# Kernel tuning notes

Measured on AMD Instinct MI355X. Metric: run time of the kernel, lower is better.

Reference implementation:

```python
import jax, jax.numpy as jnp
import numpy as np

D_MODEL = 1024
N_HEADS = 16
D_HEAD = D_MODEL // N_HEADS          # 64
ROT_DIM = D_HEAD // 2                # 32, rotary dim (lucidrains dim arg)
THETA = 10000.0
BATCH, SEQ = 4, 4096


def _rope(t):
    """lucidrains rotate_queries_or_keys with seq_dim=-2, applied to t of shape (H,B,dh,S).
    Positions run along the dh axis (size D_HEAD); rotation touches only the first
    ROT_DIM entries of the last axis (S); the rest passes through unchanged."""
    inv_freq = 1.0 / (THETA ** (jnp.arange(0, ROT_DIM, 2, dtype=jnp.float32) / ROT_DIM))  # (ROT_DIM//2,)
    pos = jnp.arange(D_HEAD, dtype=jnp.float32)                                           # (dh,)
    freqs = pos[:, None] * inv_freq[None, :]                                              # (dh, ROT_DIM//2)
    freqs = jnp.repeat(freqs, 2, axis=-1)                                                 # (dh, ROT_DIM) interleaved f0,f0,f1,f1
    cos, sin = jnp.cos(freqs), jnp.sin(freqs)                                             # broadcast over (H,B,dh,ROT_DIM)
    t_rot, t_pass = t[..., :ROT_DIM], t[..., ROT_DIM:]
    x1, x2 = t_rot[..., 0::2], t_rot[..., 1::2]
    rot_half = jnp.stack((-x2, x1), axis=-1).reshape(t_rot.shape)                         # rotate_half (adjacent pairs)
    t_rot = t_rot * cos + rot_half * sin
    return jnp.concatenate([t_rot, t_pass], axis=-1)


def setup_inputs() -> dict:
    key = jax.random.key(0)
    k1, k2, k3 = jax.random.split(key, 3)
    x = jax.random.normal(k1, (BATCH, SEQ, D_MODEL), jnp.float32)
    W = jax.random.normal(k2, (3 * D_MODEL, D_MODEL), jnp.float32) * (D_MODEL ** -0.5)  # torch Linear weight layout
    b = jax.random.normal(k3, (3 * D_MODEL,), jnp.float32) * 0.01
    return {"x": x, "W": W, "b": b}


def reference(x, W, b):
    B, S, _ = x.shape
    qkv = x @ W.T + b                                            # (B,S,3D)
    qkv = qkv.reshape(B, S, N_HEADS, 3 * D_HEAD).transpose(2, 0, 3, 1)  # (H,B,3dh,S)
    q, k, v = jnp.split(qkv, 3, axis=-2)                         # each (H,B,dh,S)
    q = _rope(q)
    k = _rope(k)
    scale = D_HEAD ** -0.5
    scores = jnp.einsum('hbds,hbes->hbde', q, k) * scale         # (H,B,dh,dh) — contracts over S
    probs = jax.nn.softmax(scores, axis=-1)
    out = jnp.einsum('hbde,hbes->hbds', probs, v)                # (H,B,dh,S)
    out = out.transpose(0, 2, 1, 3).reshape(B, S, N_HEADS * D_HEAD)  # faithful to torch transpose(1,2).reshape
    return out
```

## Files before the change

### kernel.cpp

```cpp
#include <hip/hip_runtime.h>
#include <stdint.h>

#define D_MODEL 1024
#define N_HEADS 16
#define D_HEAD  64
#define BATCH   4
#define SEQ     4096
#define BS      (BATCH*SEQ)
#define QKV_N   (3*D_MODEL)
#define HB      (N_HEADS*BATCH)

using f16x8 = __attribute__((ext_vector_type(8))) _Float16;
using f32x4 = __attribute__((ext_vector_type(4))) float;

__device__ static inline ushort f2h(float f) {
    _Float16 h = (_Float16)f; ushort u; __builtin_memcpy(&u, &h, 2); return u;
}
__device__ static inline float h2f(ushort u) {
    _Float16 h; __builtin_memcpy(&h, &u, 2); return (float)h;
}
__device__ static inline void async16(const ushort* g, ushort* l) {
    __builtin_amdgcn_global_load_lds(
        (const __attribute__((address_space(1))) void*)g,
        (__attribute__((address_space(3))) void*)l, 16, 0, 0);
}

__global__ __launch_bounds__(256)
void cvt_f16(const float* __restrict__ in, ushort* __restrict__ outp)
{
    int i = (blockIdx.x * 256 + threadIdx.x) * 8;
    float4 a = *(const float4*)(in + i);
    float4 b = *(const float4*)(in + i + 4);
    *(ushort4*)(outp + i)     = make_ushort4(f2h(a.x),f2h(a.y),f2h(a.z),f2h(a.w));
    *(ushort4*)(outp + i + 4) = make_ushort4(f2h(b.x),f2h(b.y),f2h(b.z),f2h(b.w));
}

__global__ __launch_bounds__(256)
void qkv_gemm_f16(const ushort* __restrict__ Ah, const ushort* __restrict__ Bh,
                  const float* __restrict__ bias,
                  ushort* __restrict__ qh, ushort* __restrict__ kh,
                  ushort* __restrict__ varr)
{
    __shared__ ushort sA[128 * 32];
    __shared__ ushort sB[128 * 32];
    const int t = threadIdx.x;
    const int lane = t & 63, w = t >> 6;
    const int m0 = blockIdx.y * 128, n0 = blockIdx.x * 128;

    const int ar0 = (w*2 + 0) * 16 + (lane >> 2);
    const int ar1 = (w*2 + 1) * 16 + (lane >> 2);
    const int kc  = (lane & 3) * 8;
    const ushort* gA0 = Ah + (size_t)(m0 + ar0) * D_MODEL + kc;
    const ushort* gA1 = Ah + (size_t)(m0 + ar1) * D_MODEL + kc;
    const ushort* gB0 = Bh + (size_t)(n0 + ar0) * D_MODEL + kc;
    const ushort* gB1 = Bh + (size_t)(n0 + ar1) * D_MODEL + kc;
    ushort* lA0 = &sA[(w*2 + 0) * 512];
    ushort* lA1 = &sA[(w*2 + 1) * 512];
    ushort* lB0 = &sB[(w*2 + 0) * 512];
    ushort* lB1 = &sB[(w*2 + 1) * 512];

    const int wm = (w >> 1) * 64, wn = (w & 1) * 64;
    const int fr = lane & 15, fq = (lane >> 4) * 8;

    f32x4 acc[4][4] = {};

    for (int k0 = 0; k0 < D_MODEL; k0 += 32) {
        __syncthreads();
        async16(gA0, lA0); async16(gA1, lA1);
        async16(gB0, lB0); async16(gB1, lB1);
        gA0 += 32; gA1 += 32; gB0 += 32; gB1 += 32;
        __syncthreads();

        f16x8 af[4], bf[4];
        #pragma unroll
        for (int i = 0; i < 4; ++i)
            af[i] = *(const f16x8*)&sA[(wm + i*16 + fr) * 32 + fq];
        #pragma unroll
        for (int j = 0; j < 4; ++j)
            bf[j] = *(const f16x8*)&sB[(wn + j*16 + fr) * 32 + fq];
        #pragma unroll
        for (int i = 0; i < 4; ++i)
            #pragma unroll
            for (int j = 0; j < 4; ++j)
                acc[i][j] = __builtin_amdgcn_mfma_f32_16x16x32_f16(
                                af[i], bf[j], acc[i][j], 0, 0, 0);
    }

    const int col = lane & 15, rq = (lane >> 4) * 4;
    const int cgb  = n0 + wn;
    const int h    = cgb / 192;
    const int type = (cgb % 192) / 64;
    const int b    = m0 >> 12;
    const int sb   = (m0 & 4095) + wm;

    if (type < 2) {
        ushort* dst = type ? kh : qh;
        #pragma unroll
        for (int j = 0; j < 4; ++j) {
            const int ci = j*16 + col;
            const float bj = bias[cgb + ci];
            const size_t rowoff = ((size_t)(h*4 + b)*64 + ci) * SEQ;
            #pragma unroll
            for (int i = 0; i < 4; ++i) {
                const int s0 = sb + i*16 + rq;
                *(ushort4*)&dst[rowoff + s0] = make_ushort4(
                    f2h(acc[i][j][0] + bj), f2h(acc[i][j][1] + bj),
                    f2h(acc[i][j][2] + bj), f2h(acc[i][j][3] + bj));
            }
        }
    } else {
        #pragma unroll
        for (int j = 0; j < 4; ++j) {
            const int ci = j*16 + col;
            const float bj = bias[cgb + ci];
            #pragma unroll
            for (int i = 0; i < 4; ++i) {
                const int s0 = sb + i*16 + rq;
                #pragma unroll
                for (int r = 0; r < 4; ++r)
                    varr[((size_t)(h*4 + b)*SEQ + s0 + r)*64 + ci] =
                        f2h(acc[i][j][r] + bj);
            }
        }
    }
}

__global__ __launch_bounds__(256)
void rope_f16(ushort* __restrict__ qh, ushort* __restrict__ kh)
{
    int tid = blockIdx.x * 256 + threadIdx.x;
    int m  = tid & 15;
    int ci = (tid >> 4) & 63;
    int b  = (tid >> 10) & 3;
    int h  = (tid >> 12) & 15;
    ushort* base = (tid >> 16) ? kh : qh;

    float invf = powf(10000.0f, -(float)m / 16.0f);
    float f = (float)ci * invf;
    float cs = cosf(f), sn = sinf(f);

    ushort* p = base + ((size_t)((h*4 + b)*64 + ci)) * SEQ + 2*m;
    float e0 = h2f(p[0]), e1 = h2f(p[1]);
    p[0] = f2h(e0*cs - e1*sn);
    p[1] = f2h(e1*cs + e0*sn);
}

__global__ __launch_bounds__(256)
void scores_softmax(const ushort* __restrict__ qh, const ushort* __restrict__ kh,
                    ushort* __restrict__ Pt)
{
    __shared__ float L[4 * 64 * 64];
    const int t = threadIdx.x, lane = t & 63, w = t >> 6;
    const int hb = blockIdx.x;
    const ushort* qb = qh + (size_t)hb * 64 * SEQ;
    const ushort* kb = kh + (size_t)hb * 64 * SEQ;
    const int fr = lane & 15, fq = (lane >> 4) * 8;

    f32x4 acc[4][4] = {};
    const int kbase = w * 1024;
    for (int kk = 0; kk < 1024; kk += 32) {
        const int k0 = kbase + kk;
        f16x8 af[4], bf[4];
        #pragma unroll
        for (int i = 0; i < 4; ++i)
            af[i] = *(const f16x8*)&qb[(size_t)(i*16 + fr) * SEQ + k0 + fq];
        #pragma unroll
        for (int j = 0; j < 4; ++j)
            bf[j] = *(const f16x8*)&kb[(size_t)(j*16 + fr) * SEQ + k0 + fq];
        #pragma unroll
        for (int i = 0; i < 4; ++i)
            #pragma unroll
            for (int j = 0; j < 4; ++j)
                acc[i][j] = __builtin_amdgcn_mfma_f32_16x16x32_f16(
                                af[i], bf[j], acc[i][j], 0, 0, 0);
    }

    float* Lw = &L[w * 4096];
    const int col = lane & 15, rq = (lane >> 4) * 4;
    #pragma unroll
    for (int i = 0; i < 4; ++i)
        #pragma unroll
        for (int j = 0; j < 4; ++j)
            #pragma unroll
            for (int r = 0; r < 4; ++r)
                Lw[(i*16 + rq + r)*64 + j*16 + col] = acc[i][j][r];
    __syncthreads();

    #pragma unroll
    for (int u = 0; u < 16; ++u) {
        int idx = t*16 + u;
        L[idx] = L[idx] + L[4096 + idx] + L[8192 + idx] + L[12288 + idx];
    }
    __syncthreads();

    if (t < 64) {
        float* row = &L[t * 64];
        float mx = -1e30f;
        for (int e = 0; e < 64; ++e) mx = fmaxf(mx, row[e]);
        float sum = 0.f;
        for (int e = 0; e < 64; ++e) {
            float v = expf(0.125f * (row[e] - mx));
            row[e] = v; sum += v;
        }
        float inv = 1.f / sum;
        ushort* pd = Pt + (size_t)hb * 4096 + t * 64;
        for (int e = 0; e < 64; ++e) pd[e] = f2h(row[e] * inv);
    }
}

__global__ __launch_bounds__(256)
void attn_out_mfma(const ushort* __restrict__ varr, const ushort* __restrict__ Pt,
                   float* __restrict__ out)
{
    const int t = threadIdx.x, lane = t & 63, w = t >> 6;
    const int hb = blockIdx.x;
    const int sbase = blockIdx.y * 256 + w * 64;
    const int fr = lane & 15, fq = (lane >> 4) * 8;

    const ushort* Pb = Pt + (size_t)hb * 4096;
    const ushort* vb = varr + (size_t)hb * SEQ * 64;

    f16x8 aP[4][2], bV[4][2];
    #pragma unroll
    for (int i = 0; i < 4; ++i)
        #pragma unroll
        for (int ks = 0; ks < 2; ++ks)
            aP[i][ks] = *(const f16x8*)&Pb[(i*16 + fr)*64 + ks*32 + fq];
    #pragma unroll
    for (int j = 0; j < 4; ++j)
        #pragma unroll
        for (int ks = 0; ks < 2; ++ks)
            bV[j][ks] = *(const f16x8*)&vb[(size_t)(sbase + j*16 + fr)*64 + ks*32 + fq];

    f32x4 acc[4][4] = {};
    #pragma unroll
    for (int ks = 0; ks < 2; ++ks)
        #pragma unroll
        for (int i = 0; i < 4; ++i)
            #pragma unroll
            for (int j = 0; j < 4; ++j)
                acc[i][j] = __builtin_amdgcn_mfma_f32_16x16x32_f16(
                                aP[i][ks], bV[j][ks], acc[i][j], 0, 0, 0);

    const int col = lane & 15, rq = (lane >> 4) * 4;
    const int h = hb >> 2, b = hb & 3;
    #pragma unroll
    for (int i = 0; i < 4; ++i)
        #pragma unroll
        for (int j = 0; j < 4; ++j)
            #pragma unroll
            for (int r = 0; r < 4; ++r)
                out[(((size_t)h*64 + i*16 + rq + r)*4 + b)*SEQ + sbase + j*16 + col]
                    = acc[i][j][r];
}

extern "C" void kernel_launch(void* const* d_in, const int* in_sizes, int n_in,
                              void* d_out, int out_size, void* d_ws, size_t ws_size,
                              hipStream_t stream)
{
    const float* x    = (const float*)d_in[0];
    const float* W    = (const float*)d_in[1];
    const float* bias = (const float*)d_in[2];
    float* out = (float*)d_out;

    char* p = (char*)d_ws;
    ushort* qh   = (ushort*)p;  p += (size_t)HB * 64 * SEQ * 2;
    ushort* kh   = (ushort*)p;  p += (size_t)HB * 64 * SEQ * 2;
    ushort* varr = (ushort*)p;  p += (size_t)HB * SEQ * 64 * 2;
    ushort* Pth  = (ushort*)p;  p += (size_t)HB * 4096 * 2;
    ushort* xh   = (ushort*)p;  p += (size_t)BS * D_MODEL * 2;
    ushort* Wh   = (ushort*)p;  p += (size_t)QKV_N * D_MODEL * 2;

    const int nx = BS * D_MODEL;
    const int nw = QKV_N * D_MODEL;
    cvt_f16<<<nx/2048, 256, 0, stream>>>(x, xh);
    cvt_f16<<<nw/2048, 256, 0, stream>>>(W, Wh);

    qkv_gemm_f16<<<dim3(QKV_N/128, BS/128), 256, 0, stream>>>(
        xh, Wh, bias, qh, kh, varr);

    rope_f16<<<512, 256, 0, stream>>>(qh, kh);
    scores_softmax<<<64, 256, 0, stream>>>(qh, kh, Pth);
    attn_out_mfma<<<dim3(64, 16), 256, 0, stream>>>(varr, Pth, out);
}
```

Baseline: 335.6 us.

## Split scores over sequence chunks, fuse RoPE into GEMM epilogue, merge conversions

```diff
diff --git a/kernel.cpp b/kernel.cpp
--- a/kernel.cpp
+++ b/kernel.cpp
@@ -9,6 +9,8 @@
 #define BS      (BATCH*SEQ)
 #define QKV_N   (3*D_MODEL)
 #define HB      (N_HEADS*BATCH)
+#define NCHUNK  8
+#define CH_S    (SEQ/NCHUNK)
 
 using f16x8 = __attribute__((ext_vector_type(8))) _Float16;
 using f32x4 = __attribute__((ext_vector_type(4))) float;
@@ -26,13 +28,17 @@
 }
 
 __global__ __launch_bounds__(256)
-void cvt_f16(const float* __restrict__ in, ushort* __restrict__ outp)
+void cvt_both(const float* __restrict__ x, const float* __restrict__ W,
+              ushort* __restrict__ xh, ushort* __restrict__ Wh, int nx)
 {
     int i = (blockIdx.x * 256 + threadIdx.x) * 8;
-    float4 a = *(const float4*)(in + i);
-    float4 b = *(const float4*)(in + i + 4);
-    *(ushort4*)(outp + i)     = make_ushort4(f2h(a.x),f2h(a.y),f2h(a.z),f2h(a.w));
-    *(ushort4*)(outp + i + 4) = make_ushort4(f2h(b.x),f2h(b.y),f2h(b.z),f2h(b.w));
+    const float* src; ushort* dst; int o;
+    if (i < nx) { src = x; dst = xh; o = i; }
+    else        { src = W; dst = Wh; o = i - nx; }
+    float4 a = *(const float4*)(src + o);
+    float4 b = *(const float4*)(src + o + 4);
+    *(ushort4*)(dst + o)     = make_ushort4(f2h(a.x),f2h(a.y),f2h(a.z),f2h(a.w));
+    *(ushort4*)(dst + o + 4) = make_ushort4(f2h(b.x),f2h(b.y),f2h(b.z),f2h(b.w));
 }
 
 __global__ __launch_bounds__(256)
@@ -103,9 +109,21 @@
             #pragma unroll
             for (int i = 0; i < 4; ++i) {
                 const int s0 = sb + i*16 + rq;
+                float v0 = acc[i][j][0] + bj, v1 = acc[i][j][1] + bj;
+                float v2 = acc[i][j][2] + bj, v3 = acc[i][j][3] + bj;
+                if (s0 < 32) {
+                    int mp = s0 >> 1;
+                    float if0 = powf(10000.0f, -(float)mp / 16.0f);
+                    float if1 = powf(10000.0f, -(float)(mp + 1) / 16.0f);
+                    float a0 = (float)ci * if0, a1 = (float)ci * if1;
+                    float c0 = cosf(a0), s0n = sinf(a0);
+                    float c1 = cosf(a1), s1n = sinf(a1);
+                    float n0 = v0*c0 - v1*s0n, n1 = v1*c0 + v0*s0n;
+                    float n2 = v2*c1 - v3*s1n, n3 = v3*c1 + v2*s1n;
+                    v0 = n0; v1 = n1; v2 = n2; v3 = n3;
+                }
                 *(ushort4*)&dst[rowoff + s0] = make_ushort4(
-                    f2h(acc[i][j][0] + bj), f2h(acc[i][j][1] + bj),
-                    f2h(acc[i][j][2] + bj), f2h(acc[i][j][3] + bj));
+                    f2h(v0), f2h(v1), f2h(v2), f2h(v3));
             }
         }
     } else {
@@ -126,39 +144,19 @@
 }
 
 __global__ __launch_bounds__(256)
-void rope_f16(ushort* __restrict__ qh, ushort* __restrict__ kh)
-{
-    int tid = blockIdx.x * 256 + threadIdx.x;
-    int m  = tid & 15;
-    int ci = (tid >> 4) & 63;
-    int b  = (tid >> 10) & 3;
-    int h  = (tid >> 12) & 15;
-    ushort* base = (tid >> 16) ? kh : qh;
-
-    float invf = powf(10000.0f, -(float)m / 16.0f);
-    float f = (float)ci * invf;
-    float cs = cosf(f), sn = sinf(f);
-
-    ushort* p = base + ((size_t)((h*4 + b)*64 + ci)) * SEQ + 2*m;
-    float e0 = h2f(p[0]), e1 = h2f(p[1]);
-    p[0] = f2h(e0*cs - e1*sn);
-    p[1] = f2h(e1*cs + e0*sn);
-}
-
-__global__ __launch_bounds__(256)
-void scores_softmax(const ushort* __restrict__ qh, const ushort* __restrict__ kh,
-                    ushort* __restrict__ Pt)
-{
-    __shared__ float L[4 * 64 * 64];
+void scores_partial(const ushort* __restrict__ qh, const ushort* __restrict__ kh,
+                    float* __restrict__ partial)
+{
+    __shared__ float L[4 * 4096];
     const int t = threadIdx.x, lane = t & 63, w = t >> 6;
-    const int hb = blockIdx.x;
+    const int hb = blockIdx.x, chunk = blockIdx.y;
     const ushort* qb = qh + (size_t)hb * 64 * SEQ;
     const ushort* kb = kh + (size_t)hb * 64 * SEQ;
     const int fr = lane & 15, fq = (lane >> 4) * 8;
 
     f32x4 acc[4][4] = {};
-    const int kbase = w * 1024;
-    for (int kk = 0; kk < 1024; kk += 32) {
+    const int kbase = chunk * CH_S + w * (CH_S / 4);
+    for (int kk = 0; kk < CH_S / 4; kk += 32) {
         const int k0 = kbase + kk;
         f16x8 af[4], bf[4];
         #pragma unroll
@@ -186,15 +184,38 @@
                 Lw[(i*16 + rq + r)*64 + j*16 + col] = acc[i][j][r];
     __syncthreads();
 
+    float* pb = partial + ((size_t)hb * NCHUNK + chunk) * 4096;
+    #pragma unroll
+    for (int u = 0; u < 4; ++u) {
+        int idx = u*1024 + t*4;
+        f32x4 s = *(f32x4*)&L[idx];
+        s += *(f32x4*)&L[4096 + idx];
+        s += *(f32x4*)&L[8192 + idx];
+        s += *(f32x4*)&L[12288 + idx];
+        *(f32x4*)&pb[idx] = s;
+    }
+}
+
+__global__ __launch_bounds__(256)
+void softmax_k(const float* __restrict__ partial, ushort* __restrict__ Pt)
+{
+    __shared__ float L[64 * 65];
+    const int t = threadIdx.x;
+    const int hb = blockIdx.x;
+    const float* pb = partial + (size_t)hb * NCHUNK * 4096;
+
     #pragma unroll
     for (int u = 0; u < 16; ++u) {
-        int idx = t*16 + u;
-        L[idx] = L[idx] + L[4096 + idx] + L[8192 + idx] + L[12288 + idx];
+        int idx = u*256 + t;
+        float s = 0.f;
+        #pragma unroll
+        for (int c = 0; c < NCHUNK; ++c) s += pb[c*4096 + idx];
+        L[(idx >> 6) * 65 + (idx & 63)] = s;
     }
     __syncthreads();
 
     if (t < 64) {
-        float* row = &L[t * 64];
+        float* row = &L[t * 65];
         float mx = -1e30f;
         for (int e = 0; e < 64; ++e) mx = fmaxf(mx, row[e]);
         float sum = 0.f;
@@ -214,23 +235,23 @@
 {
     const int t = threadIdx.x, lane = t & 63, w = t >> 6;
     const int hb = blockIdx.x;
-    const int sbase = blockIdx.y * 256 + w * 64;
+    const int sb = blockIdx.y * 256 + w * 64;
     const int fr = lane & 15, fq = (lane >> 4) * 8;
 
     const ushort* Pb = Pt + (size_t)hb * 4096;
     const ushort* vb = varr + (size_t)hb * SEQ * 64;
 
-    f16x8 aP[4][2], bV[4][2];
+    f16x8 aV[4][2], bP[4][2];
     #pragma unroll
     for (int i = 0; i < 4; ++i)
         #pragma unroll
         for (int ks = 0; ks < 2; ++ks)
-            aP[i][ks] = *(const f16x8*)&Pb[(i*16 + fr)*64 + ks*32 + fq];
+            aV[i][ks] = *(const f16x8*)&vb[(size_t)(sb + i*16 + fr)*64 + ks*32 + fq];
     #pragma unroll
     for (int j = 0; j < 4; ++j)
         #pragma unroll
         for (int ks = 0; ks < 2; ++ks)
-            bV[j][ks] = *(const f16x8*)&vb[(size_t)(sbase + j*16 + fr)*64 + ks*32 + fq];
+            bP[j][ks] = *(const f16x8*)&Pb[(j*16 + fr)*64 + ks*32 + fq];
 
     f32x4 acc[4][4] = {};
     #pragma unroll
@@ -240,18 +261,19 @@
             #pragma unroll
             for (int j = 0; j < 4; ++j)
                 acc[i][j] = __builtin_amdgcn_mfma_f32_16x16x32_f16(
-                                aP[i][ks], bV[j][ks], acc[i][j], 0, 0, 0);
+                                aV[i][ks], bP[j][ks], acc[i][j], 0, 0, 0);
 
     const int col = lane & 15, rq = (lane >> 4) * 4;
     const int h = hb >> 2, b = hb & 3;
     #pragma unroll
     for (int i = 0; i < 4; ++i)
         #pragma unroll
-        for (int j = 0; j < 4; ++j)
-            #pragma unroll
-            for (int r = 0; r < 4; ++r)
-                out[(((size_t)h*64 + i*16 + rq + r)*4 + b)*SEQ + sbase + j*16 + col]
-                    = acc[i][j][r];
+        for (int j = 0; j < 4; ++j) {
+            const int dg = j*16 + col;
+            size_t off = (((size_t)h*64 + dg)*4 + b)*SEQ + sb + i*16 + rq;
+            *(float4*)&out[off] = make_float4(acc[i][j][0], acc[i][j][1],
+                                              acc[i][j][2], acc[i][j][3]);
+        }
 }
 
 extern "C" void kernel_launch(void* const* d_in, const int* in_sizes, int n_in,
@@ -268,18 +290,18 @@
     ushort* kh   = (ushort*)p;  p += (size_t)HB * 64 * SEQ * 2;
     ushort* varr = (ushort*)p;  p += (size_t)HB * SEQ * 64 * 2;
     ushort* Pth  = (ushort*)p;  p += (size_t)HB * 4096 * 2;
+    float* partial = (float*)p; p += (size_t)HB * NCHUNK * 4096 * 4;
     ushort* xh   = (ushort*)p;  p += (size_t)BS * D_MODEL * 2;
     ushort* Wh   = (ushort*)p;  p += (size_t)QKV_N * D_MODEL * 2;
 
     const int nx = BS * D_MODEL;
     const int nw = QKV_N * D_MODEL;
-    cvt_f16<<<nx/2048, 256, 0, stream>>>(x, xh);
-    cvt_f16<<<nw/2048, 256, 0, stream>>>(W, Wh);
+    cvt_both<<<(nx + nw)/2048, 256, 0, stream>>>(x, W, xh, Wh, nx);
 
     qkv_gemm_f16<<<dim3(QKV_N/128, BS/128), 256, 0, stream>>>(
         xh, Wh, bias, qh, kh, varr);
 
-    rope_f16<<<512, 256, 0, stream>>>(qh, kh);
-    scores_softmax<<<64, 256, 0, stream>>>(qh, kh, Pth);
-    attn_out_mfma<<<dim3(64, 16), 256, 0, stream>>>(varr, Pth, out);
-}
+    scores_partial<<<dim3(HB, NCHUNK), 256, 0, stream>>>(qh, kh, partial);
+    softmax_k<<<HB, 256, 0, stream>>>(partial, Pth);
+    attn_out_mfma<<<dim3(HB, 16), 256, 0, stream>>>(varr, Pth, out);
+}
```

New measurement: 319.5 us. -4.8%, faster.
